# Kernel tuning notes

Hardware: AMD Instinct MI355X
Metric: run time of the kernel (lower is better)

## Reference

```python
import jax, jax.numpy as jnp
import numpy as np
import math

B, DIM, H, W = 4, 96, 64, 64
DIM3 = DIM * 3
DSTATE = 16

def _dwconv(x, w, b):
    # x: (B, d, L); torch Conv1d(k=4, pad=3, groups=d) then slice [:L] == left-pad 3
    y = jax.lax.conv_general_dilated(x, w, (1,), [(3, 0)],
                                     dimension_numbers=('NCH', 'OIH', 'NCH'),
                                     feature_group_count=x.shape[1])
    return y + b[None, :, None]

def _ln(x, g, b):
    m = jnp.mean(x, -1, keepdims=True)
    v = jnp.var(x, -1, keepdims=True)
    return (x - m) * jax.lax.rsqrt(v + 1e-5) * g + b

def _selective_scan(u, delta, A, Bs, Cs, D, z, delta_bias):
    # u, delta, z: (B, d, L); A: (d, N); Bs, Cs: (B, N, L)
    delta = jax.nn.softplus(delta + delta_bias[None, :, None])
    dT, uT = jnp.moveaxis(delta, 2, 0), jnp.moveaxis(u, 2, 0)   # (L, B, d)
    BT, CT = jnp.moveaxis(Bs, 2, 0), jnp.moveaxis(Cs, 2, 0)     # (L, B, N)
    h0 = jnp.zeros((u.shape[0], A.shape[0], A.shape[1]), u.dtype)
    def step(h, inp):
        d_t, u_t, b_t, c_t = inp
        h = jnp.exp(d_t[..., None] * A) * h + (d_t * u_t)[..., None] * b_t[:, None, :]
        return h, jnp.einsum('bdn,bn->bd', h, c_t)
    _, ys = jax.lax.scan(step, h0, (dT, uT, BT, CT))
    y = jnp.moveaxis(ys, 0, 2) + D[None, :, None] * u
    return y * jax.nn.silu(z)

def _sss(x, z_anchor, in_w, conv_w, conv_b, x_w, dt_w, dt_b, Alog, Dp, out_w):
    Bb, C, Hh, Ww = x.shape
    L = Hh * Ww
    r = dt_w.shape[0]
    xf = x.reshape(Bb, C, L).transpose(0, 2, 1) + z_anchor[:, None, :]
    x_in, z_gate = jnp.split(xf @ in_w, 2, axis=-1)
    xc = jax.nn.silu(_dwconv(x_in.transpose(0, 2, 1), conv_w, conv_b))  # (B, di, L)
    xdbl = xc.transpose(0, 2, 1) @ x_w
    dt, Bs, Cs = jnp.split(xdbl, [r, r + DSTATE], axis=-1)
    y = _selective_scan(xc, (dt @ dt_w).transpose(0, 2, 1), -jnp.exp(Alog),
                        Bs.transpose(0, 2, 1), Cs.transpose(0, 2, 1), Dp,
                        z_gate.transpose(0, 2, 1), dt_b)
    return (y.transpose(0, 2, 1) @ out_w).transpose(0, 2, 1).reshape(Bb, C, Hh, Ww)

def _sts(x, K, Q, in_w, conv_w, conv_b, kln_g, kln_b, k_w, k_b, qln_g, qln_b, q_w, q_b,
         dtbc_w, dt_w, dt_b, gate_w, gate_b, Alog, Dp, out_w):
    Bb, C, Hh, Ww = x.shape
    L = Hh * Ww
    r = dt_w.shape[0]
    xf = x.reshape(Bb, C, L).transpose(0, 2, 1)
    xc = jax.nn.silu(_dwconv((xf @ in_w).transpose(0, 2, 1), conv_w, conv_b))  # (B, di, L)
    x_t = xc.transpose(0, 2, 1)
    Kf = K.reshape(Bb, C, L).transpose(0, 2, 1)
    Qf = Q.reshape(Bb, C, L).transpose(0, 2, 1)
    K_p = jax.nn.silu(_ln(Kf, kln_g, kln_b) @ k_w + k_b)
    Q_p = jax.nn.silu(_ln(Qf, qln_g, qln_b) @ q_w + q_b)
    xdbl = jnp.concatenate([x_t, K_p], -1) @ dtbc_w
    dt, Bs, Cs = jnp.split(xdbl, [r, r + DSTATE], axis=-1)
    z_g = (jnp.concatenate([x_t, Q_p], -1) @ gate_w + gate_b).transpose(0, 2, 1)
    y = _selective_scan(xc, (dt @ dt_w).transpose(0, 2, 1), -jnp.exp(Alog),
                        Bs.transpose(0, 2, 1), Cs.transpose(0, 2, 1), Dp, z_g, dt_b)
    return (y.transpose(0, 2, 1) @ out_w).transpose(0, 2, 1).reshape(Bb, C, Hh, Ww)

def setup_inputs():
    key = jax.random.key(0)
    ks = iter(jax.random.split(key, 64))
    def nrm(shape, s=0.02):
        return jax.random.normal(next(ks), shape, jnp.float32) * s
    di, di3 = DIM * 2, DIM3 * 2
    r, r3 = math.ceil(DIM / 16), math.ceil(DIM3 / 16)
    Alog = jnp.log(jnp.tile(jnp.arange(1.0, DSTATE + 1.0, dtype=jnp.float32), (di, 1)))
    Alog3 = jnp.log(jnp.tile(jnp.arange(1.0, DSTATE + 1.0, dtype=jnp.float32), (di3, 1)))
    return dict(
        m_ll=jax.random.normal(next(ks), (B, DIM, H, W), jnp.float32),
        m_high=jax.random.normal(next(ks), (B, DIM3, H, W), jnp.float32),
        z=jax.random.normal(next(ks), (B, DIM), jnp.float32),
        K=jax.random.normal(next(ks), (B, DIM3, H, W), jnp.float32),
        Q=jax.random.normal(next(ks), (B, DIM3, H, W), jnp.float32),
        s_in_w=nrm((DIM, 2 * di)), s_conv_w=nrm((di, 1, 4), 0.2), s_conv_b=nrm((di,)),
        s_x_w=nrm((di, r + 2 * DSTATE)), s_dt_w=nrm((r, di)), s_dt_b=nrm((di,)),
        s_Alog=Alog, s_D=jnp.ones((di,), jnp.float32), s_out_w=nrm((di, DIM)),
        t_in_w=nrm((DIM3, di3)), t_conv_w=nrm((di3, 1, 4), 0.2), t_conv_b=nrm((di3,)),
        t_kln_g=jnp.ones((DIM3,), jnp.float32), t_kln_b=jnp.zeros((DIM3,), jnp.float32),
        t_k_w=nrm((DIM3, di3)), t_k_b=nrm((di3,)),
        t_qln_g=jnp.ones((DIM3,), jnp.float32), t_qln_b=jnp.zeros((DIM3,), jnp.float32),
        t_q_w=nrm((DIM3, di3)), t_q_b=nrm((di3,)),
        t_dtbc_w=nrm((2 * di3, r3 + 2 * DSTATE)), t_dt_w=nrm((r3, di3)), t_dt_b=nrm((di3,)),
        t_gate_w=nrm((2 * di3, di3)), t_gate_b=nrm((di3,)),
        t_Alog=Alog3, t_D=jnp.ones((di3,), jnp.float32), t_out_w=nrm((di3, DIM3)),
    )

def reference(m_ll, m_high, z, K, Q,
              s_in_w, s_conv_w, s_conv_b, s_x_w, s_dt_w, s_dt_b, s_Alog, s_D, s_out_w,
              t_in_w, t_conv_w, t_conv_b, t_kln_g, t_kln_b, t_k_w, t_k_b,
              t_qln_g, t_qln_b, t_q_w, t_q_b, t_dtbc_w, t_dt_w, t_dt_b,
              t_gate_w, t_gate_b, t_Alog, t_D, t_out_w):
    o1 = m_ll + _sss(m_ll, z, s_in_w, s_conv_w, s_conv_b, s_x_w, s_dt_w, s_dt_b, s_Alog, s_D, s_out_w)
    o2 = m_high + _sts(m_high, K, Q, t_in_w, t_conv_w, t_conv_b, t_kln_g, t_kln_b, t_k_w, t_k_b,
                       t_qln_g, t_qln_b, t_q_w, t_q_b, t_dtbc_w, t_dt_w, t_dt_b,
                       t_gate_w, t_gate_b, t_Alog, t_D, t_out_w)
    return (o1, o2)
```

## Files before the change

kernel.cpp:

```cpp
#include <hip/hip_runtime.h>
#include <math.h>

#define L 4096

typedef unsigned short u16;
typedef unsigned int u32;
typedef float f32x4 __attribute__((ext_vector_type(4)));
typedef short s16x8 __attribute__((ext_vector_type(8)));
typedef __attribute__((address_space(3))) unsigned int lds_u32;
typedef __attribute__((address_space(1))) unsigned int glb_u32;

__device__ __forceinline__ float softplus_f(float x) {
  return fmaxf(x, 0.f) + log1pf(__expf(-fabsf(x)));
}
__device__ __forceinline__ float silu_f(float x) {
  return x / (1.f + __expf(-x));
}
__device__ __forceinline__ float bf2f(u16 v) {
  return __uint_as_float(((unsigned)v) << 16);
}
__device__ __forceinline__ u16 f2bf(float f) {
  unsigned u = __float_as_uint(f);
  u += 0x7FFFu + ((u >> 16) & 1u);
  return (u16)(u >> 16);
}

struct WSeg { const float* src; u16* dst; int K, N, Npad; };
struct WAll { WSeg s[8]; };

__global__ __launch_bounds__(256) void wconv_k(WAll wa) {
  const WSeg w = wa.s[blockIdx.z];
  const int nb = blockIdx.x * 32, kb = blockIdx.y * 32;
  if (nb >= w.Npad || kb >= w.K) return;
  __shared__ float t[32][33];
  const int tx = threadIdx.x & 31, ty = threadIdx.x >> 5;
  for (int r = ty; r < 32; r += 8) {
    int k = kb + r, n = nb + tx;
    t[r][tx] = (n < w.N) ? w.src[(size_t)k * w.N + n] : 0.f;
  }
  __syncthreads();
  for (int r = ty; r < 32; r += 8) {
    int n = nb + r;
    w.dst[(size_t)n * w.K + kb + tx] = f2bf(t[tx][r]);
  }
}

struct TSeg { const float *x, *gam, *bet, *bias2; u16* out; int C, doLN; };
struct TPack { TSeg s[4]; };

__global__ __launch_bounds__(256) void trans_pack_k(TPack pk) {
  const TSeg t = pk.s[blockIdx.x >> 9];
  const int local = blockIdx.x & 511;
  const int C = t.C;
  __shared__ float tile[288][33];
  __shared__ float psum[8][32], psq[8][32];
  __shared__ float mm[32], rr[32];
  const int tid = threadIdx.x;
  const int l0 = (local & 127) * 32;
  const int b = local >> 7;
  const int lane32 = tid & 31, row8 = tid >> 5;
  const float* xb = t.x + (size_t)b * C * L + l0;

  for (int c = row8; c < C; c += 8)
    tile[c][lane32] = xb[(size_t)c * L + lane32];
  __syncthreads();

  if (t.doLN) {
    float s = 0.f, sq = 0.f;
    for (int c = row8; c < C; c += 8) {
      float v = tile[c][lane32];
      s += v; sq = fmaf(v, v, sq);
    }
    psum[row8][lane32] = s; psq[row8][lane32] = sq;
    __syncthreads();
    if (row8 == 0) {
      float ts = 0.f, tq = 0.f;
      #pragma unroll
      for (int g = 0; g < 8; ++g) { ts += psum[g][lane32]; tq += psq[g][lane32]; }
      float m = ts / C;
      float var = tq / C - m * m;
      mm[lane32] = m;
      rr[lane32] = rsqrtf(var + 1e-5f);
    }
    __syncthreads();
  }

  u16* ob = t.out + ((size_t)b * L + l0) * C;
  const int total = 32 * C;
  for (int o = tid * 8; o < total; o += 2048) {
    int tt = o / C, c = o % C;
    float m = 0.f, rs = 0.f;
    if (t.doLN) { m = mm[tt]; rs = rr[tt]; }
    union { u16 u[8]; int4 v; } pkv;
    #pragma unroll
    for (int j = 0; j < 8; ++j) {
      float v = tile[c + j][tt];
      if (t.doLN) v = (v - m) * rs * t.gam[c + j] + t.bet[c + j];
      else if (t.bias2) v += t.bias2[b * C + c + j];
      pkv.u[j] = f2bf(v);
    }
    *(int4*)(ob + o) = pkv.v;
  }
}

struct CSeg { const u16* x; const float* w; const float* b; u16* y; int C, nbx; };
struct CPack { CSeg s[2]; int start1; };

__global__ __launch_bounds__(256) void conv_pack_k(CPack pk) {
  const int bid = blockIdx.x;
  const int si = bid >= pk.start1;
  const CSeg q = pk.s[si];
  const int local = si ? bid - pk.start1 : bid;
  const int C = q.C;
  const int c = (local % q.nbx) * 64 + (threadIdx.x & 63);
  const int chunk = (local / q.nbx) * 4 + (threadIdx.x >> 6);
  const int T0 = chunk * 8;
  const float w0 = q.w[c * 4], w1 = q.w[c * 4 + 1], w2 = q.w[c * 4 + 2], w3 = q.w[c * 4 + 3];
  const float bs = q.b[c];
  const bool first = (T0 & (L - 1)) == 0;
  float v[11];
  #pragma unroll
  for (int i = 0; i < 11; ++i) {
    if (i < 3 && first) v[i] = 0.f;
    else v[i] = bf2f(q.x[(size_t)(T0 - 3 + i) * C + c]);
  }
  #pragma unroll
  for (int j = 0; j < 8; ++j) {
    float s = bs + w0 * v[j] + w1 * v[j + 1] + w2 * v[j + 2] + w3 * v[j + 3];
    q.y[(size_t)(T0 + j) * C + c] = f2bf(silu_f(s));
  }
}

struct MSeg {
  const u16 *A0, *A1, *Wt;
  const float *bias, *res;
  float* outF; u16 *outB0, *outB1;
  int K, K1, Nout, ldA, ldo, split, nbx, nwg, epi;
};
struct MPack { MSeg s[4]; int starts[4]; int nseg; };

__global__ __launch_bounds__(256) void mfma_pack_k(MPack pk) {
  const int bid = blockIdx.x;
  int si = 0;
  #pragma unroll
  for (int k = 1; k < 4; ++k)
    if (k < pk.nseg && bid >= pk.starts[k]) si = k;
  const MSeg p = pk.s[si];
  const int wg = bid - pk.starts[si];

  __shared__ u16 lds[16384];
  u16* As0 = lds;
  u16* Bs0 = lds + 8192;
  const int tid = threadIdx.x;
  const int lane = tid & 63;
  const int wid = tid >> 6;
  const int wm = wid >> 1, wn = wid & 1;
  const int newid = (wg & 7) * (p.nwg >> 3) + (wg >> 3);
  const int n0 = (newid % p.nbx) * 128;
  const int m0 = (newid / p.nbx) * 128;
  const int srow = tid & 127;
  const int skc = tid >> 7;
  const int kgrp = lane >> 4, l16 = lane & 15;

  f32x4 acc[4][4];
  #pragma unroll
  for (int i = 0; i < 4; ++i)
    #pragma unroll
    for (int j = 0; j < 4; ++j)
      acc[i][j] = (f32x4){0.f, 0.f, 0.f, 0.f};

  auto stage = [&](int bi, int k0) {
    const u16* Ab = p.A0;
    int kc = k0;
    if (p.A1 && k0 >= p.K1) { Ab = p.A1; kc = k0 - p.K1; }
    const u16* g0 = Ab + (size_t)(m0 + srow) * p.ldA + kc + skc * 8;
    u16* Ad = As0 + bi * 4096;
    __builtin_amdgcn_global_load_lds((const glb_u32*)g0,
        (lds_u32*)(Ad + wid * 512), 16, 0, 0);
    __builtin_amdgcn_global_load_lds((const glb_u32*)(g0 + 16),
        (lds_u32*)(Ad + 2048 + wid * 512), 16, 0, 0);
    const u16* h0 = p.Wt + (size_t)(n0 + srow) * p.K + k0 + skc * 8;
    u16* Bd = Bs0 + bi * 4096;
    __builtin_amdgcn_global_load_lds((const glb_u32*)h0,
        (lds_u32*)(Bd + wid * 512), 16, 0, 0);
    __builtin_amdgcn_global_load_lds((const glb_u32*)(h0 + 16),
        (lds_u32*)(Bd + 2048 + wid * 512), 16, 0, 0);
  };

  const int nt = p.K >> 5;
  stage(0, 0);
  __syncthreads();
  for (int t = 0; t < nt; ++t) {
    const int cur = t & 1;
    if (t + 1 < nt) stage(cur ^ 1, (t + 1) << 5);
    s16x8 af[4], bfr[4];
    #pragma unroll
    for (int mi = 0; mi < 4; ++mi)
      af[mi] = *(const s16x8*)(As0 + cur * 4096 + kgrp * 1024 + (wm * 64 + mi * 16 + l16) * 8);
    #pragma unroll
    for (int ni = 0; ni < 4; ++ni)
      bfr[ni] = *(const s16x8*)(Bs0 + cur * 4096 + kgrp * 1024 + (wn * 64 + ni * 16 + l16) * 8);
    #pragma unroll
    for (int mi = 0; mi < 4; ++mi)
      #pragma unroll
      for (int ni = 0; ni < 4; ++ni)
        acc[mi][ni] = __builtin_amdgcn_mfma_f32_16x16x32_bf16(af[mi], bfr[ni], acc[mi][ni], 0, 0, 0);
    if (t + 1 < nt) __syncthreads();
  }

  if (p.epi == 0) {
    #pragma unroll
    for (int mi = 0; mi < 4; ++mi) {
      #pragma unroll
      for (int j = 0; j < 4; ++j) {
        int token = m0 + wm * 64 + mi * 16 + (lane >> 4) * 4 + j;
        #pragma unroll
        for (int ni = 0; ni < 4; ++ni) {
          int n = n0 + wn * 64 + ni * 16 + l16;
          if (n < p.Nout) p.outF[(size_t)token * p.ldo + n] = acc[mi][ni][j];
        }
      }
    }
  } else if (p.epi == 2) {
    #pragma unroll
    for (int mi = 0; mi < 4; ++mi) {
      int token = m0 + wm * 64 + mi * 16 + (lane >> 4) * 4;
      int b = token >> 12, l = token & (L - 1);
      #pragma unroll
      for (int ni = 0; ni < 4; ++ni) {
        int n = n0 + wn * 64 + ni * 16 + l16;
        if (n < p.Nout) {
          size_t o = ((size_t)b * p.Nout + n) * L + l;
          float4 r = *(const float4*)(p.res + o);
          float4 v = make_float4(acc[mi][ni][0] + r.x, acc[mi][ni][1] + r.y,
                                 acc[mi][ni][2] + r.z, acc[mi][ni][3] + r.w);
          *(float4*)(p.outF + o) = v;
        }
      }
    }
  } else {
    __syncthreads();
    #pragma unroll
    for (int mi = 0; mi < 4; ++mi) {
      #pragma unroll
      for (int j = 0; j < 4; ++j) {
        int tok = wm * 64 + mi * 16 + (lane >> 4) * 4 + j;
        #pragma unroll
        for (int ni = 0; ni < 4; ++ni) {
          int nl = wn * 64 + ni * 16 + l16;
          int n = n0 + nl;
          float v = acc[mi][ni][j];
          if (n < p.Nout && (p.epi == 3 || p.epi == 4)) {
            v += p.bias[n];
            if (p.epi == 3) v = silu_f(v);
          }
          lds[tok * 128 + ((((nl >> 4) ^ (tok & 7))) << 4) + (nl & 15)] = f2bf(v);
        }
      }
    }
    __syncthreads();
    #pragma unroll
    for (int it = 0; it < 8; ++it) {
      int idx = it * 256 + tid;
      int row = idx >> 4, c16 = idx & 15;
      int nl0 = c16 * 8;
      if (n0 + nl0 < p.Nout) {
        int g = nl0 >> 4;
        int4 vv = *(const int4*)(lds + row * 128 + ((g ^ (row & 7)) << 4) + (nl0 & 15));
        int token = m0 + row;
        if (p.epi == 5) {
          int n = n0 + nl0;
          if (n < p.split) *(int4*)(p.outB0 + (size_t)token * p.split + n) = vv;
          else *(int4*)(p.outB1 + (size_t)token * p.split + (n - p.split)) = vv;
        } else {
          *(int4*)(p.outB0 + (size_t)token * p.ldo + n0 + nl0) = vv;
        }
      }
    }
  }
}

struct FSeg { const float* A0; const float* W; const float* eb; float* out; int K, N, lda, ldo, nbx; };
struct FPack { FSeg s[2]; int start1; };

__global__ __launch_bounds__(256) void gemm_f32_pack_k(FPack pk) {
  const int bid = blockIdx.x;
  const int si = bid >= pk.start1;
  const FSeg p = pk.s[si];
  const int local = si ? bid - pk.start1 : bid;
  const int n0 = (local % p.nbx) * 64;
  const int m0 = (local / p.nbx) * 64;

  __shared__ __align__(16) float As[16][64];
  __shared__ __align__(16) float Bs[16][64];
  const int tid = threadIdx.x;
  const int kidx = tid >> 4;
  const int li4 = (tid & 15) << 2;
  const int r0 = (tid & 15) << 2;
  const int c0 = (tid >> 4) << 2;
  float acc[4][4] = {};

  for (int k0 = 0; k0 < p.K; k0 += 16) {
    __syncthreads();
    {
      const int row = tid >> 2;
      const int kk4 = (tid & 3) << 2;
      const float* src = p.A0 + (size_t)(m0 + row) * p.lda;
      #pragma unroll
      for (int j = 0; j < 4; ++j) {
        int k = k0 + kk4 + j;
        As[kk4 + j][row] = (k < p.K) ? src[k] : 0.f;
      }
    }
    {
      int k = k0 + kidx;
      #pragma unroll
      for (int j = 0; j < 4; ++j) {
        int n = n0 + li4 + j;
        Bs[kidx][li4 + j] = (k < p.K && n < p.N) ? p.W[(size_t)k * p.N + n] : 0.f;
      }
    }
    __syncthreads();
    #pragma unroll
    for (int kk = 0; kk < 16; ++kk) {
      float4 a = *(const float4*)&As[kk][r0];
      float4 bq = *(const float4*)&Bs[kk][c0];
      float av[4] = {a.x, a.y, a.z, a.w};
      float bv[4] = {bq.x, bq.y, bq.z, bq.w};
      #pragma unroll
      for (int i = 0; i < 4; ++i)
        #pragma unroll
        for (int j = 0; j < 4; ++j)
          acc[i][j] = fmaf(av[i], bv[j], acc[i][j]);
    }
  }
  float eb[4] = {p.eb[n0 + c0], p.eb[n0 + c0 + 1], p.eb[n0 + c0 + 2], p.eb[n0 + c0 + 3]};
  #pragma unroll
  for (int i = 0; i < 4; ++i) {
    float4 v;
    v.x = softplus_f(acc[i][0] + eb[0]);
    v.y = softplus_f(acc[i][1] + eb[1]);
    v.z = softplus_f(acc[i][2] + eb[2]);
    v.w = softplus_f(acc[i][3] + eb[3]);
    *(float4*)&p.out[(size_t)(m0 + r0 + i) * p.ldo + n0 + c0] = v;
  }
}

struct S2Seg {
  const u16* u; const float* dlt; const float* Alog; const float* xdbl;
  const float* Dp; const u16* zT; float* PF; u16* yT;
  int roff, Dch, CLen, NCH;
};
struct S2Pack { S2Seg s[2]; int start1; };

template<int PASS>
__global__ __launch_bounds__(256) void scan2_pack_k(S2Pack pk) {
  const int bid = blockIdx.x;
  const int si = bid >= pk.start1;
  const S2Seg q = pk.s[si];
  const int lbid = si ? bid - pk.start1 : bid;
  const int gtid = lbid * 256 + (int)threadIdx.x;
  const int Dch = q.Dch;
  const int NC = L / q.CLen;
  const int d = gtid % Dch;
  const int c = (gtid / Dch) % NC;
  const int b = gtid / (Dch * NC);
  const size_t tok0 = (size_t)b * L + (size_t)c * q.CLen;

  float An[16], h[16];
  #pragma unroll
  for (int n = 0; n < 16; ++n) {
    An[n] = -__expf(q.Alog[d * 16 + n]);
    h[n] = 0.f;
  }
  bool fast = true;
  #pragma unroll
  for (int n = 1; n < 16; ++n) {
    float ref = (float)(n + 1) * An[0];
    if (fabsf(An[n] - ref) > 1e-4f * fabsf(ref)) fast = false;
  }

  const int ch = b * Dch + d;
  if (PASS == 3) {
    #pragma unroll
    for (int n = 0; n < 16; ++n)
      h[n] = q.PF[((size_t)c * 32 + 16 + n) * q.NCH + ch];
  }
  const float Dd = q.Dp[d];
  const u16* up = q.u + tok0 * Dch + d;
  const float* dp = q.dlt + tok0 * Dch + d;
  const u16* zp = q.zT + tok0 * Dch + d;
  u16* yr = q.yT + tok0 * Dch + d;
  const float* xr = q.xdbl + tok0 * 64 + q.roff;
  float S = 0.f;

  #define SCAN_BODY(FAST)                                                      \
  for (int t = 0; t < q.CLen; ++t) {                                           \
    const size_t od = (size_t)t * Dch;                                         \
    float dl = dp[od];                                                         \
    float uu = bf2f(up[od]);                                                   \
    float w = dl * uu;                                                         \
    const float2* bp = (const float2*)(xr + (size_t)t * 64);                   \
    float Bv[16];                                                              \
    _Pragma("unroll")                                                          \
    for (int qq = 0; qq < 8; ++qq) {                                           \
      float2 bv = bp[qq]; Bv[2 * qq] = bv.x; Bv[2 * qq + 1] = bv.y;            \
    }                                                                          \
    if (PASS == 1) S += dl;                                                    \
    float y = 0.f;                                                             \
    if (FAST) {                                                                \
      float a = __expf(dl * An[0]);                                            \
      float e = a;                                                             \
      h[0] = fmaf(e, h[0], w * Bv[0]);                                         \
      _Pragma("unroll")                                                        \
      for (int n = 1; n < 16; ++n) {                                           \
        e *= a;                                                                \
        h[n] = fmaf(e, h[n], w * Bv[n]);                                       \
      }                                                                        \
    } else {                                                                   \
      _Pragma("unroll")                                                        \
      for (int n = 0; n < 16; ++n)                                             \
        h[n] = fmaf(__expf(dl * An[n]), h[n], w * Bv[n]);                      \
    }                                                                          \
    if (PASS == 3) {                                                           \
      _Pragma("unroll")                                                        \
      for (int qq = 0; qq < 8; ++qq) {                                         \
        float2 cv = bp[qq + 8];                                                \
        y = fmaf(h[2 * qq], cv.x, y);                                          \
        y = fmaf(h[2 * qq + 1], cv.y, y);                                      \
      }                                                                        \
      float zv = bf2f(zp[od]);                                                 \
      yr[od] = f2bf((y + Dd * uu) * silu_f(zv));                               \
    }                                                                          \
  }

  if (fast) { SCAN_BODY(1) } else { SCAN_BODY(0) }
  #undef SCAN_BODY

  if (PASS == 1) {
    #pragma unroll
    for (int n = 0; n < 16; ++n) {
      q.PF[((size_t)c * 32 + n) * q.NCH + ch] = __expf(An[n] * S);
      q.PF[((size_t)c * 32 + 16 + n) * q.NCH + ch] = h[n];
    }
  }
}

__global__ __launch_bounds__(256) void stitch_pack_k(
    float* PF0, int NC0, int NCH0, int tot0,
    float* PF1, int NC1, int NCH1, int tot1) {
  int idx = blockIdx.x * 256 + threadIdx.x;
  float* PF; int NC, NCH;
  if (idx < tot0) { PF = PF0; NC = NC0; NCH = NCH0; }
  else { idx -= tot0; if (idx >= tot1) return; PF = PF1; NC = NC1; NCH = NCH1; }
  int ch = idx % NCH, n = idx / NCH;
  float hin = 0.f;
  for (int c = 0; c < NC; ++c) {
    float* Ps = PF + ((size_t)c * 32 + n) * NCH + ch;
    float* Fs = PF + ((size_t)c * 32 + 16 + n) * NCH + ch;
    float Pv = *Ps, Fv = *Fs;
    *Fs = hin;
    hin = fmaf(Pv, hin, Fv);
  }
}

extern "C" void kernel_launch(void* const* d_in, const int* in_sizes, int n_in,
                              void* d_out, int out_size, void* d_ws, size_t ws_size,
                              hipStream_t stream) {
  const float* m_ll    = (const float*)d_in[0];
  const float* m_high  = (const float*)d_in[1];
  const float* zanc    = (const float*)d_in[2];
  const float* Kin     = (const float*)d_in[3];
  const float* Qin     = (const float*)d_in[4];
  const float* s_in_w  = (const float*)d_in[5];
  const float* s_conv_w= (const float*)d_in[6];
  const float* s_conv_b= (const float*)d_in[7];
  const float* s_x_w   = (const float*)d_in[8];
  const float* s_dt_w  = (const float*)d_in[9];
  const float* s_dt_b  = (const float*)d_in[10];
  const float* s_Alog  = (const float*)d_in[11];
  const float* s_D     = (const float*)d_in[12];
  const float* s_out_w = (const float*)d_in[13];
  const float* t_in_w  = (const float*)d_in[14];
  const float* t_conv_w= (const float*)d_in[15];
  const float* t_conv_b= (const float*)d_in[16];
  const float* t_kln_g = (const float*)d_in[17];
  const float* t_kln_b = (const float*)d_in[18];
  const float* t_k_w   = (const float*)d_in[19];
  const float* t_k_b   = (const float*)d_in[20];
  const float* t_qln_g = (const float*)d_in[21];
  const float* t_qln_b = (const float*)d_in[22];
  const float* t_q_w   = (const float*)d_in[23];
  const float* t_q_b   = (const float*)d_in[24];
  const float* t_dtbc_w= (const float*)d_in[25];
  const float* t_dt_w  = (const float*)d_in[26];
  const float* t_dt_b  = (const float*)d_in[27];
  const float* t_gate_w= (const float*)d_in[28];
  const float* t_gate_b= (const float*)d_in[29];
  const float* t_Alog  = (const float*)d_in[30];
  const float* t_D     = (const float*)d_in[31];
  const float* t_out_w = (const float*)d_in[32];

  float* out1 = (float*)d_out;
  float* out2 = out1 + (size_t)4 * 96 * L;
  float* ws = (float*)d_ws;

  u16* w_sin   = (u16*)(ws + 0);
  u16* w_sx    = (u16*)(ws + 18432);
  u16* w_sout  = (u16*)(ws + 30720);
  u16* w_tin   = (u16*)(ws + 43008);
  u16* w_tk    = (u16*)(ws + 135168);
  u16* w_tq    = (u16*)(ws + 227328);
  u16* w_tdtbc = (u16*)(ws + 319488);
  u16* w_tgate = (u16*)(ws + 393216);
  u16* w_tout  = (u16*)(ws + 761856);

  float* B_ahi  = ws + 872448;
  float* B_aK   = ws + 3231744;
  float* B_aQ   = ws + 5591040;
  float* B_all  = ws + 7950336;
  float* B_xin  = ws + 8736768;
  float* B_zTs  = ws + 10309632;
  float* B_xc   = ws + 11882496;
  float* B_xin3 = ws + 13455360;
  float* B_xc3  = ws + 18173952;
  float* B_kp   = ws + 22892544;
  float* B_qp   = ws + 27611136;
  float* B_zg3  = ws + 32329728;
  float* B_xdbl = ws + 37048320;
  float* B_xdbl3= ws + 38096896;
  float* B_PFs  = ws + 39145472;
  float* B_dlt  = B_ahi;
  float* B_dlt3 = B_kp;
  u16* y_bf = (u16*)B_xin;
  u16* y3   = (u16*)B_xin3;
  float* PFt = out2;

  dim3 blk(256);

  {
    WAll wa;
    wa.s[0] = {s_in_w,   w_sin,    96, 384, 384};
    wa.s[1] = {s_x_w,    w_sx,    192,  38, 128};
    wa.s[2] = {s_out_w,  w_sout,  192,  96, 128};
    wa.s[3] = {t_in_w,   w_tin,   288, 576, 640};
    wa.s[4] = {t_k_w,    w_tk,    288, 576, 640};
    wa.s[5] = {t_q_w,    w_tq,    288, 576, 640};
    wa.s[6] = {t_dtbc_w, w_tdtbc, 1152, 50, 128};
    wa.s[7] = {t_gate_w, w_tgate, 1152, 576, 640};
    wconv_k<<<dim3(20, 36, 8), blk, 0, stream>>>(wa);
    WAll wb;
    wb.s[0] = {t_out_w,  w_tout,  576, 288, 384};
    wconv_k<<<dim3(12, 18, 1), blk, 0, stream>>>(wb);
  }

  {
    TPack tp{};
    tp.s[0] = {m_ll,   nullptr, nullptr, zanc,    (u16*)B_all, 96,  0};
    tp.s[1] = {m_high, nullptr, nullptr, nullptr, (u16*)B_ahi, 288, 0};
    tp.s[2] = {Kin,    t_kln_g, t_kln_b, nullptr, (u16*)B_aK,  288, 1};
    tp.s[3] = {Qin,    t_qln_g, t_qln_b, nullptr, (u16*)B_aQ,  288, 1};
    trans_pack_k<<<dim3(2048), blk, 0, stream>>>(tp);
  }

  {
    MPack pk{}; pk.nseg = 4;
    pk.starts[0] = 0; pk.starts[1] = 384; pk.starts[2] = 1024; pk.starts[3] = 1664;
    MSeg a{}; a.A0 = (u16*)B_all; a.Wt = w_sin; a.K = 96; a.K1 = 1 << 28; a.Nout = 384;
    a.ldA = 96; a.split = 192; a.outB0 = (u16*)B_xin; a.outB1 = (u16*)B_zTs;
    a.nbx = 3; a.nwg = 384; a.epi = 5; pk.s[0] = a;
    MSeg b{}; b.A0 = (u16*)B_ahi; b.Wt = w_tin; b.K = 288; b.K1 = 1 << 28; b.Nout = 576;
    b.ldA = 288; b.ldo = 576; b.outB0 = (u16*)B_xin3; b.nbx = 5; b.nwg = 640; b.epi = 1; pk.s[1] = b;
    MSeg c{}; c.A0 = (u16*)B_aK; c.Wt = w_tk; c.K = 288; c.K1 = 1 << 28; c.Nout = 576;
    c.ldA = 288; c.ldo = 576; c.bias = t_k_b; c.outB0 = (u16*)B_kp; c.nbx = 5; c.nwg = 640; c.epi = 3; pk.s[2] = c;
    MSeg d{}; d.A0 = (u16*)B_aQ; d.Wt = w_tq; d.K = 288; d.K1 = 1 << 28; d.Nout = 576;
    d.ldA = 288; d.ldo = 576; d.bias = t_q_b; d.outB0 = (u16*)B_qp; d.nbx = 5; d.nwg = 640; d.epi = 3; pk.s[3] = d;
    mfma_pack_k<<<dim3(2304), blk, 0, stream>>>(pk);
  }

  {
    CPack cp{}; cp.start1 = 1536;
    cp.s[0] = {(u16*)B_xin,  s_conv_w, s_conv_b, (u16*)B_xc,  192, 3};
    cp.s[1] = {(u16*)B_xin3, t_conv_w, t_conv_b, (u16*)B_xc3, 576, 9};
    conv_pack_k<<<dim3(6144), blk, 0, stream>>>(cp);
  }

  {
    MPack pk{}; pk.nseg = 3;
    pk.starts[0] = 0; pk.starts[1] = 128; pk.starts[2] = 256; pk.starts[3] = 896;
    MSeg a{}; a.A0 = (u16*)B_xc; a.Wt = w_sx; a.K = 192; a.K1 = 1 << 28; a.Nout = 64;
    a.ldA = 192; a.ldo = 64; a.outF = B_xdbl; a.nbx = 1; a.nwg = 128; a.epi = 0; pk.s[0] = a;
    MSeg b{}; b.A0 = (u16*)B_xc3; b.A1 = (u16*)B_kp; b.Wt = w_tdtbc; b.K = 1152; b.K1 = 576;
    b.Nout = 64; b.ldA = 576; b.ldo = 64; b.outF = B_xdbl3; b.nbx = 1; b.nwg = 128; b.epi = 0; pk.s[1] = b;
    MSeg c{}; c.A0 = (u16*)B_xc3; c.A1 = (u16*)B_qp; c.Wt = w_tgate; c.K = 1152; c.K1 = 576;
    c.Nout = 576; c.ldA = 576; c.ldo = 576; c.bias = t_gate_b; c.outB0 = (u16*)B_zg3;
    c.nbx = 5; c.nwg = 640; c.epi = 4; pk.s[2] = c;
    mfma_pack_k<<<dim3(896), blk, 0, stream>>>(pk);
  }

  {
    FPack fp{}; fp.start1 = 768;
    fp.s[0] = {B_xdbl,  s_dt_w, s_dt_b, B_dlt,  6,  192, 64, 192, 3};
    fp.s[1] = {B_xdbl3, t_dt_w, t_dt_b, B_dlt3, 18, 576, 64, 576, 9};
    gemm_f32_pack_k<<<dim3(3072), blk, 0, stream>>>(fp);
  }

  S2Pack sp{}; sp.start1 = 384;
  sp.s[0] = {(u16*)B_xc,  B_dlt,  s_Alog, B_xdbl,  s_D, (u16*)B_zTs, B_PFs, y_bf, 6,  192, 32, 768};
  sp.s[1] = {(u16*)B_xc3, B_dlt3, t_Alog, B_xdbl3, t_D, (u16*)B_zg3, PFt,   y3,   18, 576, 64, 2304};
  scan2_pack_k<1><<<dim3(960), blk, 0, stream>>>(sp);
  stitch_pack_k<<<dim3(192), blk, 0, stream>>>(B_PFs, 128, 768, 12288, PFt, 64, 2304, 36864);
  scan2_pack_k<3><<<dim3(960), blk, 0, stream>>>(sp);

  {
    MPack pk{}; pk.nseg = 2;
    pk.starts[0] = 0; pk.starts[1] = 128; pk.starts[2] = 512; pk.starts[3] = 512;
    MSeg a{}; a.A0 = y_bf; a.Wt = w_sout; a.K = 192; a.K1 = 1 << 28; a.Nout = 96;
    a.ldA = 192; a.res = m_ll; a.outF = out1; a.nbx = 1; a.nwg = 128; a.epi = 2; pk.s[0] = a;
    MSeg b{}; b.A0 = y3; b.Wt = w_tout; b.K = 576; b.K1 = 1 << 28; b.Nout = 288;
    b.ldA = 576; b.res = m_high; b.outF = out2; b.nbx = 3; b.nwg = 384; b.epi = 2; pk.s[1] = b;
    mfma_pack_k<<<dim3(512), blk, 0, stream>>>(pk);
  }
}
```

Before: 422.8 us.

## Stage per-chunk B/C rows in LDS and map one chunk-slice per block

Restructures the chunked selective-scan kernels so each block handles one (batch, chunk, 192-channel slice) and cooperatively loads the chunk's B (and C in pass 3) rows from xdbl into shared memory. Each thread then reads them as broadcast LDS vector loads instead of every thread re-reading the same global rows. The cost is that 64 of 256 threads sit idle during the scan, and there is an extra staging pass plus a barrier. The grid grows from 960 to 1280 blocks.

```diff
diff --git a/kernel.cpp b/kernel.cpp
--- a/kernel.cpp
+++ b/kernel.cpp
@@ -346,102 +346,111 @@
   }
 }
 
-struct S2Seg {
+struct S3Seg {
   const u16* u; const float* dlt; const float* Alog; const float* xdbl;
   const float* Dp; const u16* zT; float* PF; u16* yT;
-  int roff, Dch, CLen, NCH;
+  int roff, Dch, CLen, NCH, nsl;
 };
-struct S2Pack { S2Seg s[2]; int start1; };
+struct S3Pack { S3Seg s[2]; int start1; };
 
 template<int PASS>
-__global__ __launch_bounds__(256) void scan2_pack_k(S2Pack pk) {
+__global__ __launch_bounds__(256) void scan3_pack_k(S3Pack pk) {
+  __shared__ float rows[64][32];
   const int bid = blockIdx.x;
   const int si = bid >= pk.start1;
-  const S2Seg q = pk.s[si];
-  const int lbid = si ? bid - pk.start1 : bid;
-  const int gtid = lbid * 256 + (int)threadIdx.x;
-  const int Dch = q.Dch;
+  const S3Seg q = pk.s[si];
+  const int local = si ? bid - pk.start1 : bid;
+  const int nsl = q.nsl;
   const int NC = L / q.CLen;
-  const int d = gtid % Dch;
-  const int c = (gtid / Dch) % NC;
-  const int b = gtid / (Dch * NC);
+  const int slice = local % nsl;
+  const int c = (local / nsl) % NC;
+  const int b = local / (nsl * NC);
+  const int tid = threadIdx.x;
   const size_t tok0 = (size_t)b * L + (size_t)c * q.CLen;
 
-  float An[16], h[16];
-  #pragma unroll
-  for (int n = 0; n < 16; ++n) {
-    An[n] = -__expf(q.Alog[d * 16 + n]);
-    h[n] = 0.f;
-  }
-  bool fast = true;
-  #pragma unroll
-  for (int n = 1; n < 16; ++n) {
-    float ref = (float)(n + 1) * An[0];
-    if (fabsf(An[n] - ref) > 1e-4f * fabsf(ref)) fast = false;
-  }
-
-  const int ch = b * Dch + d;
-  if (PASS == 3) {
-    #pragma unroll
-    for (int n = 0; n < 16; ++n)
-      h[n] = q.PF[((size_t)c * 32 + 16 + n) * q.NCH + ch];
-  }
-  const float Dd = q.Dp[d];
-  const u16* up = q.u + tok0 * Dch + d;
-  const float* dp = q.dlt + tok0 * Dch + d;
-  const u16* zp = q.zT + tok0 * Dch + d;
-  u16* yr = q.yT + tok0 * Dch + d;
-  const float* xr = q.xdbl + tok0 * 64 + q.roff;
-  float S = 0.f;
-
-  #define SCAN_BODY(FAST)                                                      \
-  for (int t = 0; t < q.CLen; ++t) {                                           \
-    const size_t od = (size_t)t * Dch;                                         \
-    float dl = dp[od];                                                         \
-    float uu = bf2f(up[od]);                                                   \
-    float w = dl * uu;                                                         \
-    const float2* bp = (const float2*)(xr + (size_t)t * 64);                   \
-    float Bv[16];                                                              \
-    _Pragma("unroll")                                                          \
-    for (int qq = 0; qq < 8; ++qq) {                                           \
-      float2 bv = bp[qq]; Bv[2 * qq] = bv.x; Bv[2 * qq + 1] = bv.y;            \
-    }                                                                          \
-    if (PASS == 1) S += dl;                                                    \
-    float y = 0.f;                                                             \
-    if (FAST) {                                                                \
-      float a = __expf(dl * An[0]);                                            \
-      float e = a;                                                             \
-      h[0] = fmaf(e, h[0], w * Bv[0]);                                         \
+  const int W2 = (PASS == 1) ? 8 : 16;
+  const int tot2 = q.CLen * W2;
+  for (int i = tid; i < tot2; i += 256) {
+    int r = i / W2, j = i - r * W2;
+    float2 v = *(const float2*)(q.xdbl + (tok0 + r) * 64 + q.roff + 2 * j);
+    *(float2*)&rows[r][2 * j] = v;
+  }
+  __syncthreads();
+
+  if (tid < 192) {
+    const int d = slice * 192 + tid;
+    const int Dch = q.Dch;
+    float An[16], h[16];
+    #pragma unroll
+    for (int n = 0; n < 16; ++n) {
+      An[n] = -__expf(q.Alog[d * 16 + n]);
+      h[n] = 0.f;
+    }
+    bool fast = true;
+    #pragma unroll
+    for (int n = 1; n < 16; ++n) {
+      float ref = (float)(n + 1) * An[0];
+      if (fabsf(An[n] - ref) > 1e-4f * fabsf(ref)) fast = false;
+    }
+    const int ch = b * Dch + d;
+    if (PASS == 3) {
+      #pragma unroll
+      for (int n = 0; n < 16; ++n)
+        h[n] = q.PF[((size_t)c * 32 + 16 + n) * q.NCH + ch];
+    }
+    const float Dd = q.Dp[d];
+    const u16* up = q.u + tok0 * Dch + d;
+    const float* dp = q.dlt + tok0 * Dch + d;
+    const u16* zp = q.zT + tok0 * Dch + d;
+    u16* yr = q.yT + tok0 * Dch + d;
+    float S = 0.f;
+
+    #define SCAN_BODY(FAST)                                                    \
+    for (int t = 0; t < q.CLen; ++t) {                                         \
+      const size_t od = (size_t)t * Dch;                                       \
+      float dl = dp[od];                                                       \
+      float uu = bf2f(up[od]);                                                 \
+      float w = dl * uu;                                                       \
+      f32x4 B4[4];                                                             \
       _Pragma("unroll")                                                        \
-      for (int n = 1; n < 16; ++n) {                                           \
-        e *= a;                                                                \
-        h[n] = fmaf(e, h[n], w * Bv[n]);                                       \
+      for (int g = 0; g < 4; ++g) B4[g] = *(const f32x4*)&rows[t][4 * g];      \
+      if (PASS == 1) S += dl;                                                  \
+      float y = 0.f;                                                           \
+      if (FAST) {                                                              \
+        float a = __expf(dl * An[0]);                                          \
+        float e = a;                                                           \
+        h[0] = fmaf(e, h[0], w * B4[0][0]);                                    \
+        _Pragma("unroll")                                                      \
+        for (int n = 1; n < 16; ++n) {                                         \
+          e *= a;                                                              \
+          h[n] = fmaf(e, h[n], w * B4[n >> 2][n & 3]);                         \
+        }                                                                      \
+      } else {                                                                 \
+        _Pragma("unroll")                                                      \
+        for (int n = 0; n < 16; ++n)                                           \
+          h[n] = fmaf(__expf(dl * An[n]), h[n], w * B4[n >> 2][n & 3]);        \
       }                                                                        \
-    } else {                                                                   \
-      _Pragma("unroll")                                                        \
-      for (int n = 0; n < 16; ++n)                                             \
-        h[n] = fmaf(__expf(dl * An[n]), h[n], w * Bv[n]);                      \
-    }                                                                          \
-    if (PASS == 3) {                                                           \
-      _Pragma("unroll")                                                        \
-      for (int qq = 0; qq < 8; ++qq) {                                         \
-        float2 cv = bp[qq + 8];                                                \
-        y = fmaf(h[2 * qq], cv.x, y);                                          \
-        y = fmaf(h[2 * qq + 1], cv.y, y);                                      \
+      if (PASS == 3) {                                                         \
+        f32x4 C4[4];                                                           \
+        _Pragma("unroll")                                                      \
+        for (int g = 0; g < 4; ++g) C4[g] = *(const f32x4*)&rows[t][16 + 4 * g]; \
+        _Pragma("unroll")                                                      \
+        for (int n = 0; n < 16; ++n)                                           \
+          y = fmaf(h[n], C4[n >> 2][n & 3], y);                                \
+        float zv = bf2f(zp[od]);                                               \
+        yr[od] = f2bf((y + Dd * uu) * silu_f(zv));                             \
       }                                                                        \
-      float zv = bf2f(zp[od]);                                                 \
-      yr[od] = f2bf((y + Dd * uu) * silu_f(zv));                               \
-    }                                                                          \
-  }
-
-  if (fast) { SCAN_BODY(1) } else { SCAN_BODY(0) }
-  #undef SCAN_BODY
-
-  if (PASS == 1) {
-    #pragma unroll
-    for (int n = 0; n < 16; ++n) {
-      q.PF[((size_t)c * 32 + n) * q.NCH + ch] = __expf(An[n] * S);
-      q.PF[((size_t)c * 32 + 16 + n) * q.NCH + ch] = h[n];
+    }
+
+    if (fast) { SCAN_BODY(1) } else { SCAN_BODY(0) }
+    #undef SCAN_BODY
+
+    if (PASS == 1) {
+      #pragma unroll
+      for (int n = 0; n < 16; ++n) {
+        q.PF[((size_t)c * 32 + n) * q.NCH + ch] = __expf(An[n] * S);
+        q.PF[((size_t)c * 32 + 16 + n) * q.NCH + ch] = h[n];
+      }
     }
   }
 }
@@ -605,12 +614,12 @@
     gemm_f32_pack_k<<<dim3(3072), blk, 0, stream>>>(fp);
   }
 
-  S2Pack sp{}; sp.start1 = 384;
-  sp.s[0] = {(u16*)B_xc,  B_dlt,  s_Alog, B_xdbl,  s_D, (u16*)B_zTs, B_PFs, y_bf, 6,  192, 32, 768};
-  sp.s[1] = {(u16*)B_xc3, B_dlt3, t_Alog, B_xdbl3, t_D, (u16*)B_zg3, PFt,   y3,   18, 576, 64, 2304};
-  scan2_pack_k<1><<<dim3(960), blk, 0, stream>>>(sp);
+  S3Pack sp{}; sp.start1 = 512;
+  sp.s[0] = {(u16*)B_xc,  B_dlt,  s_Alog, B_xdbl,  s_D, (u16*)B_zTs, B_PFs, y_bf, 6,  192, 32, 768,  1};
+  sp.s[1] = {(u16*)B_xc3, B_dlt3, t_Alog, B_xdbl3, t_D, (u16*)B_zg3, PFt,   y3,   18, 576, 64, 2304, 3};
+  scan3_pack_k<1><<<dim3(1280), blk, 0, stream>>>(sp);
   stitch_pack_k<<<dim3(192), blk, 0, stream>>>(B_PFs, 128, 768, 12288, PFt, 64, 2304, 36864);
-  scan2_pack_k<3><<<dim3(960), blk, 0, stream>>>(sp);
+  scan3_pack_k<3><<<dim3(1280), blk, 0, stream>>>(sp);
 
   {
     MPack pk{}; pk.nseg = 2;
```

Result: faster. 397.5 us, median of 2 (-6.0%).
